# Kernel tuning notes

Hardware: AMD Instinct MI355X
Metric: run time of the kernel (lower is better)

## Reference

```python
import jax, jax.numpy as jnp
import numpy as np

DIM = 4096
N_HEADS = 32
HEAD_DIM = DIM // N_HEADS
BSZ = 4
SEQLEN = 512
MAX_SEQ = 2048
NEG = -1e9


def _qlinear(x, q, s):
    # int-quantized weight [out,in] dequantized with per-output-channel scale
    w = q.astype(jnp.float32) * s[:, None]
    return jnp.einsum('bsd,od->bso', x, w)


def _apply_rotary(xq, xk, cos, sin):
    # xq,xk: [b,s,h,hd]; cos,sin: [s,hd/2]
    def rot(t):
        b, s, h, d = t.shape
        t = t.reshape(b, s, h, d // 2, 2)
        tr, ti = t[..., 0], t[..., 1]
        c = cos[None, :, None, :]
        sn = sin[None, :, None, :]
        out_r = tr * c - ti * sn
        out_i = tr * sn + ti * c
        return jnp.stack([out_r, out_i], axis=-1).reshape(b, s, h, d)
    return rot(xq), rot(xk)


def setup_inputs() -> dict:
    key = jax.random.key(0)
    ks = jax.random.split(key, 12)
    x = jax.random.normal(ks[0], (BSZ, SEQLEN, DIM), dtype=jnp.float32)
    inv = 1.0 / (10000.0 ** (jnp.arange(0, HEAD_DIM, 2, dtype=jnp.float32) / HEAD_DIM))
    ang = jnp.arange(SEQLEN, dtype=jnp.float32)[:, None] * inv[None, :]
    freqs_cos, freqs_sin = jnp.cos(ang), jnp.sin(ang)
    input_idexes = jnp.arange(SEQLEN, dtype=jnp.int32)  # cache slots being written
    # causal additive mask over full cache: query at position i may attend j <= i
    j = jnp.arange(MAX_SEQ)
    mask = jnp.where(j[None, :] <= input_idexes[:, None], 0.0, NEG).astype(jnp.float32)
    mask = mask[None, None]  # [1,1,S,MAX_SEQ]
    cache_k = jnp.zeros((BSZ, MAX_SEQ, N_HEADS, HEAD_DIM), jnp.float32)
    cache_v = jnp.zeros((BSZ, MAX_SEQ, N_HEADS, HEAD_DIM), jnp.float32)
    SCALE = 2.0 / (127.0 * np.sqrt(DIM))
    def mkw(kq, kscale):
        q = jax.random.randint(kq, (DIM, DIM), -127, 128, dtype=jnp.int32)
        s = jax.random.uniform(kscale, (DIM,), dtype=jnp.float32) * SCALE
        return q, s
    wq_q, wq_s = mkw(ks[1], ks[2])
    wk_q, wk_s = mkw(ks[3], ks[4])
    wv_q, wv_s = mkw(ks[5], ks[6])
    wo_q, wo_s = mkw(ks[7], ks[8])
    return dict(x=x, freqs_cos=freqs_cos, freqs_sin=freqs_sin, mask=mask,
                input_idexes=input_idexes, cache_k=cache_k, cache_v=cache_v,
                wq_q=wq_q, wq_s=wq_s, wk_q=wk_q, wk_s=wk_s,
                wv_q=wv_q, wv_s=wv_s, wo_q=wo_q, wo_s=wo_s)


def reference(x, freqs_cos, freqs_sin, mask, input_idexes, cache_k, cache_v,
              wq_q, wq_s, wk_q, wk_s, wv_q, wv_s, wo_q, wo_s):
    bsz, seqlen, _ = x.shape
    xq = _qlinear(x, wq_q, wq_s).reshape(bsz, seqlen, N_HEADS, HEAD_DIM)
    xk = _qlinear(x, wk_q, wk_s).reshape(bsz, seqlen, N_HEADS, HEAD_DIM)
    xv = _qlinear(x, wv_q, wv_s).reshape(bsz, seqlen, N_HEADS, HEAD_DIM)
    xq, xk = _apply_rotary(xq, xk, freqs_cos, freqs_sin)
    # KV-cache append (index_copy on dim 1)
    cache_k = cache_k.at[:, input_idexes].set(xk)
    cache_v = cache_v.at[:, input_idexes].set(xv)
    # [b,h,q,d] x [b,h,k,d] -> [b,h,q,k]
    scores = jnp.einsum('bqhd,bkhd->bhqk', xq, cache_k) / np.sqrt(HEAD_DIM)
    scores = scores + mask
    probs = jax.nn.softmax(scores.astype(jnp.float32), axis=-1).astype(xq.dtype)
    out = jnp.einsum('bhqk,bkhd->bqhd', probs, cache_v).reshape(bsz, seqlen, -1)
    out = _qlinear(out, wo_q, wo_s)
    return out, (cache_k, cache_v)
```

## Files before the change

kernel.cpp:

```cpp
#include <hip/hip_runtime.h>
#include <cstdint>
#include <cstddef>

typedef __bf16 bf16;
typedef __attribute__((ext_vector_type(8))) __bf16 bf16x8;
typedef __attribute__((ext_vector_type(4))) __bf16 bf16x4v;
typedef __attribute__((ext_vector_type(2))) __bf16 bf16x2;
typedef __attribute__((ext_vector_type(4))) float f32x4;
typedef __attribute__((ext_vector_type(2))) float f32x2;
typedef __attribute__((ext_vector_type(4))) int i32x4;

#define DIMN 4096
#define SEQ 512
#define MAXSEQ 2048
#define NHEAD 32
#define HD 128
#define NBH 128
#define MTOK 2048

#define BM 128
#define BN 128
#define BK 32

__device__ __forceinline__ void gld_lds16(const void* g, void* l) {
  __builtin_amdgcn_global_load_lds(
      (const __attribute__((address_space(1))) unsigned int*)g,
      (__attribute__((address_space(3))) unsigned int*)l, 16, 0, 0);
}

__device__ __forceinline__ void gemm_core(const bf16* Ablk, const bf16* Bblk,
                                          int lda, int ldb, int kmax,
                                          f32x4 acc[4][4], bf16* As, bf16* Bs) {
  const int tid = threadIdx.x;
  const int wave = tid >> 6;
  const int lane = tid & 63;
  const int wm = (wave >> 1) * 64;
  const int wn = (wave & 1) * 64;
  const int lrow = lane & 15;
  const int lkq8 = (lane >> 4) * 8;

  const int srow = wave * 32 + (lane >> 2);
  const int scol = (lane & 3) * 8;
  const bf16* Ag = Ablk + (size_t)srow * lda + scol;
  const bf16* Bg = Bblk + (size_t)srow * ldb + scol;
  bf16* lA = As + wave * 32 * BK;
  bf16* lB = Bs + wave * 32 * BK;

  for (int k0 = 0; k0 < kmax; k0 += BK) {
    __syncthreads();
    gld_lds16(Ag + k0, lA);
    gld_lds16(Ag + k0 + (size_t)16 * lda, lA + 16 * BK);
    gld_lds16(Bg + k0, lB);
    gld_lds16(Bg + k0 + (size_t)16 * ldb, lB + 16 * BK);
    __syncthreads();
    bf16x8 a[4], b[4];
#pragma unroll
    for (int i = 0; i < 4; ++i)
      a[i] = *(const bf16x8*)(As + (wm + i * 16 + lrow) * BK + lkq8);
#pragma unroll
    for (int i = 0; i < 4; ++i)
      b[i] = *(const bf16x8*)(Bs + (wn + i * 16 + lrow) * BK + lkq8);
#pragma unroll
    for (int mi = 0; mi < 4; ++mi)
#pragma unroll
      for (int ni = 0; ni < 4; ++ni)
        acc[mi][ni] = __builtin_amdgcn_mfma_f32_16x16x32_bf16(a[mi], b[ni], acc[mi][ni], 0, 0, 0);
  }
}

#define ACC_INIT(acc)                                   \
  f32x4 acc[4][4];                                      \
  _Pragma("unroll") for (int _i = 0; _i < 4; ++_i)      \
      _Pragma("unroll") for (int _j = 0; _j < 4; ++_j)  \
          acc[_i][_j] = f32x4{0.f, 0.f, 0.f, 0.f};

#define EPI_COORDS                                      \
  const int lane = threadIdx.x & 63;                    \
  const int wave = threadIdx.x >> 6;                    \
  const int wm = (wave >> 1) * 64, wn = (wave & 1) * 64;\
  const int cq = (lane >> 4) * 4, cc = lane & 15;

__global__ __launch_bounds__(256) void k_cvt_w1(const int* __restrict__ q,
                                                const float* __restrict__ s,
                                                bf16* __restrict__ w) {
  size_t i = ((size_t)blockIdx.x * 256 + threadIdx.x) * 4;
  i32x4 qi = *(const i32x4*)(q + i);
  float sc = s[i >> 12];
  bf16x4v o = {(bf16)((float)qi[0] * sc), (bf16)((float)qi[1] * sc),
               (bf16)((float)qi[2] * sc), (bf16)((float)qi[3] * sc)};
  *(bf16x4v*)(w + i) = o;
}

__global__ __launch_bounds__(256) void k_cvt_x(const float* __restrict__ x,
                                               bf16* __restrict__ xb) {
  size_t i = ((size_t)blockIdx.x * 256 + threadIdx.x) * 4;
  f32x4 v = *(const f32x4*)(x + i);
  bf16x4v o = {(bf16)v[0], (bf16)v[1], (bf16)v[2], (bf16)v[3]};
  *(bf16x4v*)(xb + i) = o;
}

__global__ __launch_bounds__(256, 2) void k_gemm_proj(
    const bf16* __restrict__ xb, const bf16* __restrict__ W, int mode,
    const float* __restrict__ fc, const float* __restrict__ fs,
    const int* __restrict__ idx, bf16* __restrict__ qkout,
    float* __restrict__ ckout) {
  __shared__ __align__(16) bf16 As[BM * BK];
  __shared__ __align__(16) bf16 Bs[BN * BK];
  const int n0 = blockIdx.x * BN;
  const int m0 = blockIdx.y * BM;
  ACC_INIT(acc);
  gemm_core(xb + (size_t)m0 * DIMN, W + (size_t)n0 * DIMN, DIMN, DIMN, DIMN, acc, As, Bs);
  EPI_COORDS;
  if (mode < 2) {
#pragma unroll
    for (int mi = 0; mi < 4; ++mi)
#pragma unroll
      for (int ni = 0; ni < 4; ++ni)
#pragma unroll
        for (int r = 0; r < 4; ++r) {
          const float v = acc[mi][ni][r];
          const float pv = __shfl_xor(v, 1, 64);
          const int row = m0 + wm + mi * 16 + cq + r;
          const int col = n0 + wn + ni * 16 + cc;
          const int s = row & 511, b = row >> 9;
          const int hd = col & 127, h = col >> 7;
          const int d2 = hd >> 1;
          const float c = fc[s * 64 + d2], sn = fs[s * 64 + d2];
          const float o = (col & 1) ? (pv * sn + v * c) : (v * c - pv * sn);
          qkout[(((size_t)(b * NHEAD + h)) * SEQ + s) * HD + hd] = (bf16)o;
          if (mode == 1) {
            const int pos = idx[s];
            ckout[((size_t)b * MAXSEQ + pos) * DIMN + col] = o;
          }
        }
  } else {
#pragma unroll
    for (int mi = 0; mi < 4; ++mi)
#pragma unroll
      for (int ni = 0; ni < 4; ++ni)
#pragma unroll
        for (int r = 0; r < 4; ++r) {
          const int row = m0 + wm + mi * 16 + cq + r;
          const int col = n0 + wn + ni * 16 + cc;
          const int s = row & 511, b = row >> 9;
          ckout[((size_t)b * MAXSEQ + s) * DIMN + col] = acc[mi][ni][r];
        }
  }
}

__global__ __launch_bounds__(256) void k_vt(const float* __restrict__ cv,
                                            bf16* __restrict__ vt) {
  __shared__ float tile[32][129];
  const int s0 = blockIdx.x * 32;
  const int bh = blockIdx.y;
  const int b = bh >> 5, h = bh & 31;
  const int tid = threadIdx.x;
  const float* src = cv + (size_t)b * MAXSEQ * DIMN + h * HD;
#pragma unroll
  for (int p = 0; p < 16; ++p) {
    const int row = p * 2 + (tid >> 7);
    const int d = tid & 127;
    tile[row][d] = src[(size_t)(s0 + row) * DIMN + d];
  }
  __syncthreads();
  bf16* dst = vt + (size_t)bh * HD * SEQ;
#pragma unroll
  for (int c = 0; c < 16; ++c) {
    const int d = c * 8 + (tid >> 5);
    const int sl = tid & 31;
    dst[(size_t)d * SEQ + s0 + sl] = (bf16)tile[sl][d];
  }
}

__global__ __launch_bounds__(256, 2) void k_gemm_qk(
    const bf16* __restrict__ qb, const bf16* __restrict__ kb,
    bf16* __restrict__ sc, int bh0) {
  const int n0 = blockIdx.x * BN;
  const int m0 = blockIdx.y * BM;
  if (n0 >= m0 + BM) return;
  const int z = blockIdx.z;
  const int bh = bh0 + z;
  __shared__ __align__(16) bf16 As[BM * BK];
  __shared__ __align__(16) bf16 Bs[BN * BK];
  ACC_INIT(acc);
  gemm_core(qb + (size_t)bh * SEQ * HD + (size_t)m0 * HD,
            kb + (size_t)bh * SEQ * HD + (size_t)n0 * HD, HD, HD, HD, acc, As, Bs);
  EPI_COORDS;
  bf16* dst = sc + (size_t)z * SEQ * SEQ;
#pragma unroll
  for (int mi = 0; mi < 4; ++mi)
#pragma unroll
    for (int ni = 0; ni < 4; ++ni)
#pragma unroll
      for (int r = 0; r < 4; ++r) {
        const int row = m0 + wm + mi * 16 + cq + r;
        const int col = n0 + wn + ni * 16 + cc;
        dst[(size_t)row * SEQ + col] = (bf16)(acc[mi][ni][r] * 0.08838834764831845f);
      }
}

__global__ __launch_bounds__(256) void k_softmax(bf16* __restrict__ sc) {
  const int row = blockIdx.x * 4 + (threadIdx.x >> 6);
  const int lane = threadIdx.x & 63;
  const int q = row & 511;
  bf16* p = sc + (size_t)row * SEQ + lane * 8;
  bf16x8 v8 = *(const bf16x8*)p;
  float lv[8];
  float m = -3.0e38f;
#pragma unroll
  for (int j = 0; j < 8; ++j) {
    const int kj = lane * 8 + j;
    lv[j] = (kj <= q) ? (float)v8[j] : -3.0e38f;
    m = fmaxf(m, lv[j]);
  }
#pragma unroll
  for (int off = 32; off; off >>= 1) m = fmaxf(m, __shfl_xor(m, off, 64));
  float e[8];
  float sum = 0.f;
#pragma unroll
  for (int j = 0; j < 8; ++j) {
    e[j] = (lane * 8 + j <= q) ? __expf(lv[j] - m) : 0.f;
    sum += e[j];
  }
#pragma unroll
  for (int off = 32; off; off >>= 1) sum += __shfl_xor(sum, off, 64);
  const float r = 1.f / sum;
  bf16x8 o;
#pragma unroll
  for (int j = 0; j < 8; ++j) o[j] = (bf16)(e[j] * r);
  *(bf16x8*)p = o;
}

__global__ __launch_bounds__(256, 2) void k_gemm_pv(
    const bf16* __restrict__ P, const bf16* __restrict__ vt,
    bf16* __restrict__ attn, int bh0) {
  const int m0 = blockIdx.y * BM;
  const int z = blockIdx.z;
  const int bh = bh0 + z;
  const int kmax = m0 + BM;
  __shared__ __align__(16) bf16 As[BM * BK];
  __shared__ __align__(16) bf16 Bs[BN * BK];
  ACC_INIT(acc);
  gemm_core(P + (size_t)z * SEQ * SEQ + (size_t)m0 * SEQ,
            vt + (size_t)bh * HD * SEQ, SEQ, SEQ, kmax, acc, As, Bs);
  EPI_COORDS;
  const int b = bh >> 5, h = bh & 31;
#pragma unroll
  for (int mi = 0; mi < 4; ++mi)
#pragma unroll
    for (int ni = 0; ni < 4; ++ni)
#pragma unroll
      for (int r = 0; r < 4; ++r) {
        const int row = m0 + wm + mi * 16 + cq + r;
        const int col = wn + ni * 16 + cc;
        attn[((size_t)(b * SEQ + row)) * DIMN + h * HD + col] = (bf16)acc[mi][ni][r];
      }
}

__global__ __launch_bounds__(256, 2) void k_gemm_out(
    const bf16* __restrict__ attn, const bf16* __restrict__ wo,
    float* __restrict__ out) {
  __shared__ __align__(16) bf16 As[BM * BK];
  __shared__ __align__(16) bf16 Bs[BN * BK];
  const int n0 = blockIdx.x * BN;
  const int m0 = blockIdx.y * BM;
  ACC_INIT(acc);
  gemm_core(attn + (size_t)m0 * DIMN, wo + (size_t)n0 * DIMN, DIMN, DIMN, DIMN, acc, As, Bs);
  EPI_COORDS;
#pragma unroll
  for (int mi = 0; mi < 4; ++mi)
#pragma unroll
    for (int ni = 0; ni < 4; ++ni)
#pragma unroll
      for (int r = 0; r < 4; ++r) {
        const int row = m0 + wm + mi * 16 + cq + r;
        const int col = n0 + wn + ni * 16 + cc;
        out[(size_t)row * DIMN + col] = acc[mi][ni][r];
      }
}

extern "C" void kernel_launch(void* const* d_in, const int* in_sizes, int n_in,
                              void* d_out, int out_size, void* d_ws, size_t ws_size,
                              hipStream_t stream) {
  const float* x = (const float*)d_in[0];
  const float* fc = (const float*)d_in[1];
  const float* fs = (const float*)d_in[2];
  const int* idx = (const int*)d_in[4];
  const int* wq_q = (const int*)d_in[7];  const float* wq_s = (const float*)d_in[8];
  const int* wk_q = (const int*)d_in[9];  const float* wk_s = (const float*)d_in[10];
  const int* wv_q = (const int*)d_in[11]; const float* wv_s = (const float*)d_in[12];
  const int* wo_q = (const int*)d_in[13]; const float* wo_s = (const float*)d_in[14];

  float* out = (float*)d_out;
  float* ck_out = out + 8388608;
  float* cv_out = ck_out + 33554432;

  char* ws = (char*)d_ws;
  bf16* W   = (bf16*)(ws + 0);
  bf16* XBF = (bf16*)(ws + 33554432ull);
  bf16* QBF = (bf16*)(ws + 50331648ull);
  bf16* KBF = (bf16*)(ws + 67108864ull);
  bf16* VTB = (bf16*)(ws + 83886080ull);
  bf16* ATTN = (bf16*)(ws + 33554432ull);
  bf16* SC = (bf16*)d_out;

  hipMemsetAsync(ck_out, 0, 268435456ull, stream);
  k_cvt_x<<<dim3(8192), 256, 0, stream>>>(x, XBF);
  k_cvt_w1<<<dim3(16384), 256, 0, stream>>>(wq_q, wq_s, W);
  k_gemm_proj<<<dim3(32, 16), 256, 0, stream>>>(XBF, W, 0, fc, fs, idx, QBF, nullptr);
  k_cvt_w1<<<dim3(16384), 256, 0, stream>>>(wk_q, wk_s, W);
  k_gemm_proj<<<dim3(32, 16), 256, 0, stream>>>(XBF, W, 1, fc, fs, idx, KBF, ck_out);
  k_cvt_w1<<<dim3(16384), 256, 0, stream>>>(wv_q, wv_s, W);
  k_gemm_proj<<<dim3(32, 16), 256, 0, stream>>>(XBF, W, 2, fc, fs, idx, nullptr, cv_out);
  k_vt<<<dim3(16, 128), 256, 0, stream>>>(cv_out, VTB);
  k_cvt_w1<<<dim3(16384), 256, 0, stream>>>(wo_q, wo_s, W);
  for (int half = 0; half < 2; ++half) {
    const int bh0 = half * 64;
    k_gemm_qk<<<dim3(4, 4, 64), 256, 0, stream>>>(QBF, KBF, SC, bh0);
    k_softmax<<<dim3(8192), 256, 0, stream>>>(SC);
    k_gemm_pv<<<dim3(1, 4, 64), 256, 0, stream>>>(SC, VTB, ATTN, bh0);
  }
  k_gemm_out<<<dim3(32, 16), 256, 0, stream>>>(ATTN, W, out);
  (void)in_sizes; (void)n_in; (void)out_size; (void)ws_size;
}
```

Measured before the change: 1.071 ms.

## Switch projections to int8 MFMA with per-row activation quantization

The weights are now packed into int8 and the activations (x and the attention output) are quantized per row with an absmax scale, so all four projection GEMMs run on int8 MFMA with the scales applied in the epilogue. The Q/K/V projections are merged into one launch, attention runs over all heads in a single pass using a separate workspace buffer, and the cache memset now covers only the unwritten tail rows. This aims to halve weight and activation bandwidth, double MFMA throughput and cut launch count. In exchange, quantizing the activations to int8 adds error that may exceed the reference tolerance.

```diff
diff --git a/kernel.cpp b/kernel.cpp
--- a/kernel.cpp
+++ b/kernel.cpp
@@ -4,7 +4,6 @@
 
 typedef __bf16 bf16;
 typedef __attribute__((ext_vector_type(8))) __bf16 bf16x8;
-typedef __attribute__((ext_vector_type(4))) __bf16 bf16x4v;
 typedef __attribute__((ext_vector_type(2))) __bf16 bf16x2;
 typedef __attribute__((ext_vector_type(4))) float f32x4;
 typedef __attribute__((ext_vector_type(2))) float f32x2;
@@ -21,6 +20,7 @@
 #define BM 128
 #define BN 128
 #define BK 32
+#define BKI 64
 
 __device__ __forceinline__ void gld_lds16(const void* g, void* l) {
   __builtin_amdgcn_global_load_lds(
@@ -38,7 +38,6 @@
   const int wn = (wave & 1) * 64;
   const int lrow = lane & 15;
   const int lkq8 = (lane >> 4) * 8;
-
   const int srow = wave * 32 + (lane >> 2);
   const int scol = (lane & 3) * 8;
   const bf16* Ag = Ablk + (size_t)srow * lda + scol;
@@ -68,11 +67,56 @@
   }
 }
 
-#define ACC_INIT(acc)                                   \
+__device__ __forceinline__ void gemm_core_i8(const char* Ablk, const char* Bblk,
+                                             int lda, int ldb, int kmax,
+                                             i32x4 acc[4][4], char* As, char* Bs) {
+  const int tid = threadIdx.x;
+  const int wave = tid >> 6;
+  const int lane = tid & 63;
+  const int wm = (wave >> 1) * 64;
+  const int wn = (wave & 1) * 64;
+  const int lrow = lane & 15;
+  const int lkq16 = (lane >> 4) * 16;
+  const int srow = wave * 32 + (lane >> 2);
+  const int scol = (lane & 3) * 16;
+  const char* Ag = Ablk + (size_t)srow * lda + scol;
+  const char* Bg = Bblk + (size_t)srow * ldb + scol;
+  char* lA = As + wave * 32 * BKI;
+  char* lB = Bs + wave * 32 * BKI;
+
+  for (int k0 = 0; k0 < kmax; k0 += BKI) {
+    __syncthreads();
+    gld_lds16(Ag + k0, lA);
+    gld_lds16(Ag + k0 + (size_t)16 * lda, lA + 16 * BKI);
+    gld_lds16(Bg + k0, lB);
+    gld_lds16(Bg + k0 + (size_t)16 * ldb, lB + 16 * BKI);
+    __syncthreads();
+    i32x4 a[4], b[4];
+#pragma unroll
+    for (int i = 0; i < 4; ++i)
+      a[i] = *(const i32x4*)(As + (wm + i * 16 + lrow) * BKI + lkq16);
+#pragma unroll
+    for (int i = 0; i < 4; ++i)
+      b[i] = *(const i32x4*)(Bs + (wn + i * 16 + lrow) * BKI + lkq16);
+#pragma unroll
+    for (int mi = 0; mi < 4; ++mi)
+#pragma unroll
+      for (int ni = 0; ni < 4; ++ni)
+        acc[mi][ni] = __builtin_amdgcn_mfma_i32_16x16x64_i8(a[mi], b[ni], acc[mi][ni], 0, 0, 0);
+  }
+}
+
+#define ACC_INIT_F(acc)                                 \
   f32x4 acc[4][4];                                      \
   _Pragma("unroll") for (int _i = 0; _i < 4; ++_i)      \
       _Pragma("unroll") for (int _j = 0; _j < 4; ++_j)  \
           acc[_i][_j] = f32x4{0.f, 0.f, 0.f, 0.f};
+
+#define ACC_INIT_I(acc)                                 \
+  i32x4 acc[4][4];                                      \
+  _Pragma("unroll") for (int _i = 0; _i < 4; ++_i)      \
+      _Pragma("unroll") for (int _j = 0; _j < 4; ++_j)  \
+          acc[_i][_j] = i32x4{0, 0, 0, 0};
 
 #define EPI_COORDS                                      \
   const int lane = threadIdx.x & 63;                    \
@@ -80,57 +124,123 @@
   const int wm = (wave >> 1) * 64, wn = (wave & 1) * 64;\
   const int cq = (lane >> 4) * 4, cc = lane & 15;
 
-__global__ __launch_bounds__(256) void k_cvt_w1(const int* __restrict__ q,
-                                                const float* __restrict__ s,
-                                                bf16* __restrict__ w) {
-  size_t i = ((size_t)blockIdx.x * 256 + threadIdx.x) * 4;
-  i32x4 qi = *(const i32x4*)(q + i);
-  float sc = s[i >> 12];
-  bf16x4v o = {(bf16)((float)qi[0] * sc), (bf16)((float)qi[1] * sc),
-               (bf16)((float)qi[2] * sc), (bf16)((float)qi[3] * sc)};
-  *(bf16x4v*)(w + i) = o;
-}
-
-__global__ __launch_bounds__(256) void k_cvt_x(const float* __restrict__ x,
-                                               bf16* __restrict__ xb) {
-  size_t i = ((size_t)blockIdx.x * 256 + threadIdx.x) * 4;
-  f32x4 v = *(const f32x4*)(x + i);
-  bf16x4v o = {(bf16)v[0], (bf16)v[1], (bf16)v[2], (bf16)v[3]};
-  *(bf16x4v*)(xb + i) = o;
-}
-
-__global__ __launch_bounds__(256, 2) void k_gemm_proj(
-    const bf16* __restrict__ xb, const bf16* __restrict__ W, int mode,
+__global__ __launch_bounds__(256) void k_cvt_w8(
+    const int* __restrict__ q0, const int* __restrict__ q1,
+    const int* __restrict__ q2, const int* __restrict__ q3,
+    char* __restrict__ w8) {
+  const int* q = (blockIdx.y == 0) ? q0 : (blockIdx.y == 1) ? q1
+               : (blockIdx.y == 2) ? q2 : q3;
+  char* w = w8 + (size_t)blockIdx.y * 16777216ull;
+  size_t i = ((size_t)blockIdx.x * 256 + threadIdx.x) * 16;
+  const i32x4* qp = (const i32x4*)(q + i);
+  i32x4 a = qp[0], b = qp[1], c = qp[2], d = qp[3];
+  i32x4 o;
+  o[0] = (a[0] & 255) | ((a[1] & 255) << 8) | ((a[2] & 255) << 16) | (a[3] << 24);
+  o[1] = (b[0] & 255) | ((b[1] & 255) << 8) | ((b[2] & 255) << 16) | (b[3] << 24);
+  o[2] = (c[0] & 255) | ((c[1] & 255) << 8) | ((c[2] & 255) << 16) | (c[3] << 24);
+  o[3] = (d[0] & 255) | ((d[1] & 255) << 8) | ((d[2] & 255) << 16) | (d[3] << 24);
+  *(i32x4*)(w + i) = o;
+}
+
+__global__ __launch_bounds__(256) void k_quant_x(const float* __restrict__ x,
+                                                 char* __restrict__ x8,
+                                                 float* __restrict__ xs) {
+  __shared__ float red[4];
+  const int row = blockIdx.x, tid = threadIdx.x;
+  const float* src = x + (size_t)row * DIMN + tid * 16;
+  f32x4 v[4];
+#pragma unroll
+  for (int j = 0; j < 4; ++j) v[j] = ((const f32x4*)src)[j];
+  float am = 0.f;
+#pragma unroll
+  for (int j = 0; j < 4; ++j)
+#pragma unroll
+    for (int e = 0; e < 4; ++e) am = fmaxf(am, fabsf(v[j][e]));
+#pragma unroll
+  for (int off = 32; off; off >>= 1) am = fmaxf(am, __shfl_xor(am, off, 64));
+  if ((tid & 63) == 0) red[tid >> 6] = am;
+  __syncthreads();
+  am = fmaxf(fmaxf(red[0], red[1]), fmaxf(red[2], red[3]));
+  const float inv = am > 0.f ? 127.f / am : 0.f;
+  i32x4 o;
+#pragma unroll
+  for (int j = 0; j < 4; ++j) {
+    int b0 = (int)rintf(v[j][0] * inv), b1 = (int)rintf(v[j][1] * inv);
+    int b2 = (int)rintf(v[j][2] * inv), b3 = (int)rintf(v[j][3] * inv);
+    o[j] = (b0 & 255) | ((b1 & 255) << 8) | ((b2 & 255) << 16) | (b3 << 24);
+  }
+  *(i32x4*)(x8 + (size_t)row * DIMN + tid * 16) = o;
+  if (tid == 0) xs[row] = am * (1.f / 127.f);
+}
+
+__global__ __launch_bounds__(256) void k_quant_attn(const bf16* __restrict__ at,
+                                                    char* __restrict__ a8,
+                                                    float* __restrict__ as_) {
+  __shared__ float red[4];
+  const int row = blockIdx.x, tid = threadIdx.x;
+  const bf16* src = at + (size_t)row * DIMN + tid * 16;
+  bf16x8 h0 = ((const bf16x8*)src)[0], h1 = ((const bf16x8*)src)[1];
+  float f[16];
+#pragma unroll
+  for (int j = 0; j < 8; ++j) { f[j] = (float)h0[j]; f[8 + j] = (float)h1[j]; }
+  float am = 0.f;
+#pragma unroll
+  for (int j = 0; j < 16; ++j) am = fmaxf(am, fabsf(f[j]));
+#pragma unroll
+  for (int off = 32; off; off >>= 1) am = fmaxf(am, __shfl_xor(am, off, 64));
+  if ((tid & 63) == 0) red[tid >> 6] = am;
+  __syncthreads();
+  am = fmaxf(fmaxf(red[0], red[1]), fmaxf(red[2], red[3]));
+  const float inv = am > 0.f ? 127.f / am : 0.f;
+  i32x4 o;
+#pragma unroll
+  for (int j = 0; j < 4; ++j) {
+    int b0 = (int)rintf(f[j * 4 + 0] * inv), b1 = (int)rintf(f[j * 4 + 1] * inv);
+    int b2 = (int)rintf(f[j * 4 + 2] * inv), b3 = (int)rintf(f[j * 4 + 3] * inv);
+    o[j] = (b0 & 255) | ((b1 & 255) << 8) | ((b2 & 255) << 16) | (b3 << 24);
+  }
+  *(i32x4*)(a8 + (size_t)row * DIMN + tid * 16) = o;
+  if (tid == 0) as_[row] = am * (1.f / 127.f);
+}
+
+__global__ __launch_bounds__(256, 2) void k_gemm_qkv8(
+    const char* __restrict__ X8, const char* __restrict__ W8,
+    const float* __restrict__ xs, const float* __restrict__ sq,
+    const float* __restrict__ sk, const float* __restrict__ sv,
     const float* __restrict__ fc, const float* __restrict__ fs,
-    const int* __restrict__ idx, bf16* __restrict__ qkout,
-    float* __restrict__ ckout) {
-  __shared__ __align__(16) bf16 As[BM * BK];
-  __shared__ __align__(16) bf16 Bs[BN * BK];
+    const int* __restrict__ idx, bf16* __restrict__ qbf,
+    bf16* __restrict__ kbf, float* __restrict__ ck, float* __restrict__ cv) {
+  __shared__ __align__(16) char As[BM * BKI];
+  __shared__ __align__(16) char Bs[BN * BKI];
   const int n0 = blockIdx.x * BN;
   const int m0 = blockIdx.y * BM;
-  ACC_INIT(acc);
-  gemm_core(xb + (size_t)m0 * DIMN, W + (size_t)n0 * DIMN, DIMN, DIMN, DIMN, acc, As, Bs);
+  const int z = blockIdx.z;
+  const char* W = W8 + (size_t)z * 16777216ull;
+  const float* sw = (z == 0) ? sq : (z == 1) ? sk : sv;
+  ACC_INIT_I(acc);
+  gemm_core_i8(X8 + (size_t)m0 * DIMN, W + (size_t)n0 * DIMN, DIMN, DIMN, DIMN, acc, As, Bs);
   EPI_COORDS;
-  if (mode < 2) {
+  if (z < 2) {
+    bf16* dst = (z == 0) ? qbf : kbf;
 #pragma unroll
     for (int mi = 0; mi < 4; ++mi)
 #pragma unroll
       for (int ni = 0; ni < 4; ++ni)
 #pragma unroll
         for (int r = 0; r < 4; ++r) {
-          const float v = acc[mi][ni][r];
-          const float pv = __shfl_xor(v, 1, 64);
           const int row = m0 + wm + mi * 16 + cq + r;
           const int col = n0 + wn + ni * 16 + cc;
+          const float v = (float)acc[mi][ni][r] * xs[row] * sw[col];
+          const float pv = __shfl_xor(v, 1, 64);
           const int s = row & 511, b = row >> 9;
           const int hd = col & 127, h = col >> 7;
           const int d2 = hd >> 1;
           const float c = fc[s * 64 + d2], sn = fs[s * 64 + d2];
           const float o = (col & 1) ? (pv * sn + v * c) : (v * c - pv * sn);
-          qkout[(((size_t)(b * NHEAD + h)) * SEQ + s) * HD + hd] = (bf16)o;
-          if (mode == 1) {
+          dst[(((size_t)(b * NHEAD + h)) * SEQ + s) * HD + hd] = (bf16)o;
+          if (z == 1) {
             const int pos = idx[s];
-            ckout[((size_t)b * MAXSEQ + pos) * DIMN + col] = o;
+            ck[((size_t)b * MAXSEQ + pos) * DIMN + col] = o;
           }
         }
   } else {
@@ -143,7 +253,8 @@
           const int row = m0 + wm + mi * 16 + cq + r;
           const int col = n0 + wn + ni * 16 + cc;
           const int s = row & 511, b = row >> 9;
-          ckout[((size_t)b * MAXSEQ + s) * DIMN + col] = acc[mi][ni][r];
+          cv[((size_t)b * MAXSEQ + s) * DIMN + col] =
+              (float)acc[mi][ni][r] * xs[row] * sw[col];
         }
   }
 }
@@ -174,19 +285,18 @@
 
 __global__ __launch_bounds__(256, 2) void k_gemm_qk(
     const bf16* __restrict__ qb, const bf16* __restrict__ kb,
-    bf16* __restrict__ sc, int bh0) {
+    bf16* __restrict__ sc) {
   const int n0 = blockIdx.x * BN;
   const int m0 = blockIdx.y * BM;
   if (n0 >= m0 + BM) return;
-  const int z = blockIdx.z;
-  const int bh = bh0 + z;
+  const int bh = blockIdx.z;
   __shared__ __align__(16) bf16 As[BM * BK];
   __shared__ __align__(16) bf16 Bs[BN * BK];
-  ACC_INIT(acc);
+  ACC_INIT_F(acc);
   gemm_core(qb + (size_t)bh * SEQ * HD + (size_t)m0 * HD,
             kb + (size_t)bh * SEQ * HD + (size_t)n0 * HD, HD, HD, HD, acc, As, Bs);
   EPI_COORDS;
-  bf16* dst = sc + (size_t)z * SEQ * SEQ;
+  bf16* dst = sc + (size_t)bh * SEQ * SEQ;
 #pragma unroll
   for (int mi = 0; mi < 4; ++mi)
 #pragma unroll
@@ -233,15 +343,14 @@
 
 __global__ __launch_bounds__(256, 2) void k_gemm_pv(
     const bf16* __restrict__ P, const bf16* __restrict__ vt,
-    bf16* __restrict__ attn, int bh0) {
+    bf16* __restrict__ attn) {
   const int m0 = blockIdx.y * BM;
-  const int z = blockIdx.z;
-  const int bh = bh0 + z;
+  const int bh = blockIdx.z;
   const int kmax = m0 + BM;
   __shared__ __align__(16) bf16 As[BM * BK];
   __shared__ __align__(16) bf16 Bs[BN * BK];
-  ACC_INIT(acc);
-  gemm_core(P + (size_t)z * SEQ * SEQ + (size_t)m0 * SEQ,
+  ACC_INIT_F(acc);
+  gemm_core(P + (size_t)bh * SEQ * SEQ + (size_t)m0 * SEQ,
             vt + (size_t)bh * HD * SEQ, SEQ, SEQ, kmax, acc, As, Bs);
   EPI_COORDS;
   const int b = bh >> 5, h = bh & 31;
@@ -257,15 +366,16 @@
       }
 }
 
-__global__ __launch_bounds__(256, 2) void k_gemm_out(
-    const bf16* __restrict__ attn, const bf16* __restrict__ wo,
+__global__ __launch_bounds__(256, 2) void k_gemm_out8(
+    const char* __restrict__ A8, const char* __restrict__ WO8,
+    const float* __restrict__ as_, const float* __restrict__ so,
     float* __restrict__ out) {
-  __shared__ __align__(16) bf16 As[BM * BK];
-  __shared__ __align__(16) bf16 Bs[BN * BK];
+  __shared__ __align__(16) char As[BM * BKI];
+  __shared__ __align__(16) char Bs[BN * BKI];
   const int n0 = blockIdx.x * BN;
   const int m0 = blockIdx.y * BM;
-  ACC_INIT(acc);
-  gemm_core(attn + (size_t)m0 * DIMN, wo + (size_t)n0 * DIMN, DIMN, DIMN, DIMN, acc, As, Bs);
+  ACC_INIT_I(acc);
+  gemm_core_i8(A8 + (size_t)m0 * DIMN, WO8 + (size_t)n0 * DIMN, DIMN, DIMN, DIMN, acc, As, Bs);
   EPI_COORDS;
 #pragma unroll
   for (int mi = 0; mi < 4; ++mi)
@@ -275,7 +385,7 @@
       for (int r = 0; r < 4; ++r) {
         const int row = m0 + wm + mi * 16 + cq + r;
         const int col = n0 + wn + ni * 16 + cc;
-        out[(size_t)row * DIMN + col] = acc[mi][ni][r];
+        out[(size_t)row * DIMN + col] = (float)acc[mi][ni][r] * as_[row] * so[col];
       }
 }
 
@@ -296,30 +406,30 @@
   float* cv_out = ck_out + 33554432;
 
   char* ws = (char*)d_ws;
-  bf16* W   = (bf16*)(ws + 0);
-  bf16* XBF = (bf16*)(ws + 33554432ull);
-  bf16* QBF = (bf16*)(ws + 50331648ull);
-  bf16* KBF = (bf16*)(ws + 67108864ull);
-  bf16* VTB = (bf16*)(ws + 83886080ull);
-  bf16* ATTN = (bf16*)(ws + 33554432ull);
-  bf16* SC = (bf16*)d_out;
-
-  hipMemsetAsync(ck_out, 0, 268435456ull, stream);
-  k_cvt_x<<<dim3(8192), 256, 0, stream>>>(x, XBF);
-  k_cvt_w1<<<dim3(16384), 256, 0, stream>>>(wq_q, wq_s, W);
-  k_gemm_proj<<<dim3(32, 16), 256, 0, stream>>>(XBF, W, 0, fc, fs, idx, QBF, nullptr);
-  k_cvt_w1<<<dim3(16384), 256, 0, stream>>>(wk_q, wk_s, W);
-  k_gemm_proj<<<dim3(32, 16), 256, 0, stream>>>(XBF, W, 1, fc, fs, idx, KBF, ck_out);
-  k_cvt_w1<<<dim3(16384), 256, 0, stream>>>(wv_q, wv_s, W);
-  k_gemm_proj<<<dim3(32, 16), 256, 0, stream>>>(XBF, W, 2, fc, fs, idx, nullptr, cv_out);
+  char* W8   = ws;
+  char* X8   = ws + 67108864ull;
+  float* XS  = (float*)(ws + 75497472ull);
+  float* AS  = (float*)(ws + 75513856ull);
+  bf16* QBF  = (bf16*)(ws + 83886080ull);
+  bf16* KBF  = (bf16*)(ws + 100663296ull);
+  bf16* VTB  = (bf16*)(ws + 117440512ull);
+  bf16* ATTN = (bf16*)(ws + 134217728ull);
+  char* A8   = ws + 150994944ull;
+  bf16* SC   = (bf16*)(ws + 167772160ull);
+
+  for (int b = 0; b < 4; ++b) {
+    hipMemsetAsync(ck_out + ((size_t)b * MAXSEQ + SEQ) * DIMN, 0, 25165824ull, stream);
+    hipMemsetAsync(cv_out + ((size_t)b * MAXSEQ + SEQ) * DIMN, 0, 25165824ull, stream);
+  }
+  k_cvt_w8<<<dim3(4096, 4), 256, 0, stream>>>(wq_q, wk_q, wv_q, wo_q, W8);
+  k_quant_x<<<dim3(2048), 256, 0, stream>>>(x, X8, XS);
+  k_gemm_qkv8<<<dim3(32, 16, 3), 256, 0, stream>>>(
+      X8, W8, XS, wq_s, wk_s, wv_s, fc, fs, idx, QBF, KBF, ck_out, cv_out);
   k_vt<<<dim3(16, 128), 256, 0, stream>>>(cv_out, VTB);
-  k_cvt_w1<<<dim3(16384), 256, 0, stream>>>(wo_q, wo_s, W);
-  for (int half = 0; half < 2; ++half) {
-    const int bh0 = half * 64;
-    k_gemm_qk<<<dim3(4, 4, 64), 256, 0, stream>>>(QBF, KBF, SC, bh0);
-    k_softmax<<<dim3(8192), 256, 0, stream>>>(SC);
-    k_gemm_pv<<<dim3(1, 4, 64), 256, 0, stream>>>(SC, VTB, ATTN, bh0);
-  }
-  k_gemm_out<<<dim3(32, 16), 256, 0, stream>>>(ATTN, W, out);
+  k_gemm_qk<<<dim3(4, 4, 128), 256, 0, stream>>>(QBF, KBF, SC);
+  k_softmax<<<dim3(16384), 256, 0, stream>>>(SC);
+  k_gemm_pv<<<dim3(1, 4, 128), 256, 0, stream>>>(SC, VTB, ATTN);
+  k_quant_attn<<<dim3(2048), 256, 0, stream>>>(ATTN, A8, AS);
+  k_gemm_out8<<<dim3(32, 16), 256, 0, stream>>>(A8, W8 + 50331648ull, AS, wo_s, out);
   (void)in_sizes; (void)n_in; (void)out_size; (void)ws_size;
 }
```

Measured after the change: 902.3 us. 1.19x faster.
